# Kernel optimization log

Measured on AMD Instinct MI355X. Metric: run time of the kernel, lower is better.

Reference implementation:

```python
import jax, jax.numpy as jnp
import numpy as np

NUM_HEADS = 16
ROPE_BASE = 10000.0


def _rope_tables(head_dim, seq_len, dtype=jnp.float32):
    # Half-split convention: rotate first half against second half.
    inv_freq = 1.0 / (ROPE_BASE ** (jnp.arange(0, head_dim, 2, dtype=dtype) / head_dim))
    pos = jnp.arange(seq_len, dtype=dtype)
    angles_half = jnp.einsum('s,d->sd', pos, inv_freq)          # (S, D/2)
    angles = jnp.concatenate([angles_half, angles_half], -1)     # (S, D)
    return jnp.cos(angles), jnp.sin(angles)


def _apply_rope(x, cos, sin):
    # x: (H, S, D); cos/sin: (S, D) broadcast over heads
    half = x.shape[-1] // 2
    x1, x2 = x[..., :half], x[..., half:]
    x_rot = jnp.concatenate([-x2, x1], axis=-1)
    return x * cos + x_rot * sin


def setup_inputs() -> dict:
    key = jax.random.key(0)
    S, E = 2048, 2048
    ks = jax.random.split(key, 9)
    sc = 0.02
    return {
        'x': jax.random.normal(ks[0], (S, E), jnp.float32),
        'Wq': jax.random.normal(ks[1], (E, E), jnp.float32) * sc,
        'bq': jax.random.normal(ks[2], (E,), jnp.float32) * sc,
        'Wk': jax.random.normal(ks[3], (E, E), jnp.float32) * sc,
        'bk': jax.random.normal(ks[4], (E,), jnp.float32) * sc,
        'Wv': jax.random.normal(ks[5], (E, E), jnp.float32) * sc,
        'bv': jax.random.normal(ks[6], (E,), jnp.float32) * sc,
        'Wo': jax.random.normal(ks[7], (E, E), jnp.float32) * sc,
        'bo': jax.random.normal(ks[8], (E,), jnp.float32) * sc,
    }


def reference(x, Wq, bq, Wk, bk, Wv, bv, Wo, bo):
    S, E = x.shape
    H = NUM_HEADS
    D = E // H
    scale = D ** 0.5
    cos, sin = _rope_tables(D, S, x.dtype)

    def proj(W, b):
        return (x @ W.T + b).reshape(S, H, D).transpose(1, 0, 2)  # (H, S, D)

    q = _apply_rope(proj(Wq, bq), cos, sin)
    k = _apply_rope(proj(Wk, bk), cos, sin)
    v = proj(Wv, bv)

    scores = jnp.einsum('hsd,htd->hst', q, k) / scale  # (H, S, S)
    attn = jax.nn.softmax(scores, axis=-1)
    out = jnp.einsum('hst,htd->hsd', attn, v)          # (H, S, D)
    # Faithful to the original's transpose(0,1).view(S,E) on a (1,H,S,D)
    # tensor: an in-order (head-major) flatten reinterpreted as (S, E).
    out = out.reshape(S, E)
    return out @ Wo.T + bo
```

## Files before the change

kernel.cpp:

```cpp
#include <hip/hip_runtime.h>

#define SDIM 2048
#define EDIM 2048
#define NHEAD 16
#define DHEAD 128

typedef __attribute__((ext_vector_type(8))) short short8;
typedef __attribute__((ext_vector_type(4))) float floatx4;

__device__ __forceinline__ float bf2f(ushort u) {
    union { uint i; float f; } v; v.i = ((uint)u) << 16; return v.f;
}
__device__ __forceinline__ ushort f2bf(float f) {
    union { float f; uint i; } v; v.f = f;
    uint r = v.i + 0x7fff + ((v.i >> 16) & 1);
    return (ushort)(r >> 16);
}

__device__ __forceinline__ void gload_lds16(const ushort* g, ushort* l) {
    __builtin_amdgcn_global_load_lds(
        (const __attribute__((address_space(1))) void*)g,
        (__attribute__((address_space(3))) void*)l, 16, 0, 0);
}

__global__ void convert5_kernel(
    const float* __restrict__ s0, const float* __restrict__ s1,
    const float* __restrict__ s2, const float* __restrict__ s3,
    const float* __restrict__ s4,
    ushort* __restrict__ d0, ushort* __restrict__ d1,
    ushort* __restrict__ d2, ushort* __restrict__ d3,
    ushort* __restrict__ d4)
{
    const float* src; ushort* dst;
    switch (blockIdx.y) {
        case 0: src = s0; dst = d0; break;
        case 1: src = s1; dst = d1; break;
        case 2: src = s2; dst = d2; break;
        case 3: src = s3; dst = d3; break;
        default: src = s4; dst = d4; break;
    }
    int i = blockIdx.x * blockDim.x + threadIdx.x;
    float4 f = ((const float4*)src)[i];
    ushort4 o;
    o.x = f2bf(f.x); o.y = f2bf(f.y); o.z = f2bf(f.z); o.w = f2bf(f.w);
    ((ushort4*)dst)[i] = o;
}

#define QPRESCALE 0.12754245f

__global__ __launch_bounds__(512, 2) void gemm256_qkv(
    const ushort* __restrict__ A,
    const ushort* __restrict__ B0, const ushort* __restrict__ B1, const ushort* __restrict__ B2,
    const float* __restrict__ s0, const float* __restrict__ s1, const float* __restrict__ s2,
    ushort* __restrict__ C0, ushort* __restrict__ C1, ushort* __restrict__ Vtg)
{
    __shared__ __align__(16) ushort smem[2][2][2][128 * 64];

    const int tid  = threadIdx.x;
    const int lane = tid & 63;
    const int wave = tid >> 6;
    const int l15 = lane & 15, quad = lane >> 4, l7 = lane & 7;
    const int wm = wave & 1, wn = wave >> 1;
    const int bm = blockIdx.x * 256;
    const int which = blockIdx.y >> 3;
    const int n0 = (blockIdx.y & 7) * 256;
    const int NT = EDIM / 64;

    const ushort* Bsel = (which == 0) ? B0 : (which == 1) ? B1 : B2;
    const float*  bia  = (which == 0) ? s0 : (which == 1) ? s1 : s2;

    const int srow = tid >> 3;
    const int sgc  = (((tid & 7) ^ ((tid >> 3) & 7)) << 3);

    floatx4 acc[8][4];
#pragma unroll
    for (int i = 0; i < 8; i++)
#pragma unroll
        for (int j = 0; j < 4; j++) acc[i][j] = (floatx4)0.0f;

    auto stageA = [&](int tile, int h) {
        const ushort* g = A + (size_t)(bm + h * 128 + srow) * EDIM + tile * 64 + sgc;
        ushort* l = &smem[tile & 1][0][h][0] + tid * 8;
        gload_lds16(g, l);
        gload_lds16(g + (size_t)64 * EDIM, l + 4096);
    };
    auto stageB = [&](int tile, int h) {
        const ushort* g = Bsel + (size_t)(n0 + h * 128 + srow) * EDIM + tile * 64 + sgc;
        ushort* l = &smem[tile & 1][1][h][0] + tid * 8;
        gload_lds16(g, l);
        gload_lds16(g + (size_t)64 * EDIM, l + 4096);
    };

    stageA(0, 0); stageA(0, 1); stageB(0, 0); stageB(0, 1);
    stageB(1, 0); stageB(1, 1);
    asm volatile("s_waitcnt vmcnt(4)" ::: "memory");
    __builtin_amdgcn_s_barrier();

    const int c0 = ((quad ^ l7) << 3);
    const int c1 = (((quad + 4) ^ l7) << 3);
    const int brow0 = (wn & 1) * 64;

    short8 af[4], b0[4], b1[4];

#define MFMA16(AOFF, AF, BF) \
    _Pragma("unroll") \
    for (int mf = 0; mf < 4; mf++) \
        _Pragma("unroll") \
        for (int an = 0; an < 4; an++) \
            acc[(AOFF) + mf][an] = __builtin_amdgcn_mfma_f32_16x16x32_bf16( \
                AF[mf], BF[an], acc[(AOFF) + mf][an], 0, 0, 0);

#define PH_PRE() do { \
    asm volatile("" ::: "memory"); \
    __builtin_amdgcn_s_barrier(); \
    asm volatile("s_waitcnt lgkmcnt(0)" ::: "memory"); \
    __builtin_amdgcn_sched_barrier(0); \
    __builtin_amdgcn_s_setprio(1); \
} while (0)
#define PH_POST() do { \
    __builtin_amdgcn_s_setprio(0); \
    asm volatile("" ::: "memory"); \
    __builtin_amdgcn_s_barrier(); \
} while (0)

    for (int t = 0; t < NT; ++t) {
        const ushort* aH = &smem[t & 1][0][wm][0];
        const ushort* bH = &smem[t & 1][1][wn >> 1][0];

#pragma unroll
        for (int mf = 0; mf < 4; mf++)
            af[mf] = *(const short8*)(aH + (mf * 16 + l15) * 64 + c0);
#pragma unroll
        for (int an = 0; an < 4; an++)
            b0[an] = *(const short8*)(bH + (brow0 + an * 16 + l15) * 64 + c0);
        if (t + 1 < NT) stageA(t + 1, 0);
        PH_PRE();
        MFMA16(0, af, b0);
        PH_POST();

        short8 ag[4];
#pragma unroll
        for (int mf = 0; mf < 4; mf++)
            ag[mf] = *(const short8*)(aH + (mf * 16 + l15) * 64 + c1);
#pragma unroll
        for (int an = 0; an < 4; an++)
            b1[an] = *(const short8*)(bH + (brow0 + an * 16 + l15) * 64 + c1);
        if (t + 1 < NT) stageA(t + 1, 1);
        PH_PRE();
        MFMA16(0, ag, b1);
        PH_POST();

#pragma unroll
        for (int mf = 0; mf < 4; mf++)
            af[mf] = *(const short8*)(aH + (64 + mf * 16 + l15) * 64 + c0);
        if (t + 2 < NT) stageB(t + 2, 0);
        PH_PRE();
        MFMA16(4, af, b0);
        PH_POST();

#pragma unroll
        for (int mf = 0; mf < 4; mf++)
            ag[mf] = *(const short8*)(aH + (64 + mf * 16 + l15) * 64 + c1);
        if (t + 2 < NT) stageB(t + 2, 1);
        asm volatile("" ::: "memory");
        __builtin_amdgcn_s_barrier();
        asm volatile("s_waitcnt lgkmcnt(0)" ::: "memory");
        __builtin_amdgcn_sched_barrier(0);
        __builtin_amdgcn_s_setprio(1);
        MFMA16(4, ag, b1);
        __builtin_amdgcn_s_setprio(0);
        if (t < NT - 2) asm volatile("s_waitcnt vmcnt(4)" ::: "memory");
        else            asm volatile("s_waitcnt vmcnt(0)" ::: "memory");
        __builtin_amdgcn_s_barrier();
    }
#undef MFMA16
#undef PH_PRE
#undef PH_POST

    if (which == 2) {
#pragma unroll
        for (int an = 0; an < 4; an++) {
            int col = n0 + wn * 64 + an * 16 + l15;
            int h = col >> 7, d = col & 127;
            float bv = bia[col];
            ushort* cp = Vtg + (size_t)h * SDIM * DHEAD + (size_t)d * SDIM;
#pragma unroll
            for (int am = 0; am < 8; am++) {
                int s = bm + wm * 128 + am * 16 + quad * 4;
                ushort4 pk;
                pk.x = f2bf(acc[am][an][0] + bv);
                pk.y = f2bf(acc[am][an][1] + bv);
                pk.z = f2bf(acc[am][an][2] + bv);
                pk.w = f2bf(acc[am][an][3] + bv);
                *(ushort4*)(cp + s) = pk;
            }
        }
    } else {
        ushort* C = (which == 0) ? C0 : C1;
        const float psc = (which == 0) ? QPRESCALE : 1.0f;
        float* xch = (float*)smem;
        float bv[4], invf[4];
#pragma unroll
        for (int an = 0; an < 4; an++) {
            bv[an]   = bia[n0 + wn * 64 + an * 16 + l15];
            invf[an] = __expf((float)(an * 16 + l15) * -0.14391157f);
        }
        const int mybase = wave * 1024 + quad * 16 + l15;
        const int pbase  = (wave ^ 2) * 1024 + quad * 16 + l15;
        const int rowb = bm + wm * 128 + quad * 4;
#pragma unroll
        for (int am2 = 0; am2 < 4; am2++) {
            __syncthreads();
#pragma unroll
            for (int sl = 0; sl < 2; sl++) {
                int am = am2 * 2 + sl;
#pragma unroll
                for (int an = 0; an < 4; an++)
#pragma unroll
                    for (int r = 0; r < 4; r++)
                        xch[sl * 8192 + mybase + an * 256 + r * 64] = acc[am][an][r] + bv[an];
            }
            __syncthreads();
#pragma unroll
            for (int sl = 0; sl < 2; sl++) {
                int am = am2 * 2 + sl;
#pragma unroll
                for (int an = 0; an < 4; an++) {
                    int col = n0 + wn * 64 + an * 16 + l15;
#pragma unroll
                    for (int r = 0; r < 4; r++) {
                        int row = rowb + am * 16 + r;
                        float v = acc[am][an][r] + bv[an];
                        float w = xch[sl * 8192 + pbase + an * 256 + r * 64];
                        float ang = (float)row * invf[an];
                        float rev = ang * 0.15915494309f;
                        rev -= floorf(rev);
                        float arad = rev * 6.28318530718f;
                        float sn = __sinf(arad), cs = __cosf(arad);
                        float o = ((wn & 1) == 0) ? (v * cs - w * sn) : (v * cs + w * sn);
                        C[(size_t)row * EDIM + col] = f2bf(o * psc);
                    }
                }
            }
        }
    }
}

template <typename OUTT, int KSPLIT>
__global__ __launch_bounds__(256) void gemm_bt(
    const ushort* __restrict__ A,
    const ushort* __restrict__ B0, const ushort* __restrict__ B1, const ushort* __restrict__ B2,
    const float* __restrict__ s0, const float* __restrict__ s1, const float* __restrict__ s2,
    OUTT* __restrict__ C0, OUTT* __restrict__ C1, OUTT* __restrict__ C2,
    int nbpm)
{
    __shared__ __align__(16) ushort smem[2 * 128 * 32];
    ushort* a_s = smem;
    ushort* b_s = smem + 128 * 32;

    const int tid = threadIdx.x;
    const int wave = tid >> 6, lane = tid & 63;
    const int l15 = lane & 15, quad = lane >> 4;
    const int wm = wave & 1, wn = wave >> 1;
    const int bm = blockIdx.x * 128;
    const int which = blockIdx.y / nbpm;
    const int n0 = (blockIdx.y % nbpm) * 128;

    const ushort* B;
    const float*  bia;
    OUTT*         C;
    const ushort* Abase;
    if constexpr (KSPLIT == 2) {
        B = B0; bia = s0; C = C0;
        Abase = A + which * (EDIM / 2);
    } else {
        B   = (which == 0) ? B0 : (which == 1) ? B1 : B2;
        bia = (which == 0) ? s0 : (which == 1) ? s1 : s2;
        C   = (which == 0) ? C0 : (which == 1) ? C1 : C2;
        Abase = A;
    }
    const ushort* Bbase = (KSPLIT == 2) ? B + which * (EDIM / 2) : B;

    floatx4 acc[4][4];
#pragma unroll
    for (int i = 0; i < 4; i++)
#pragma unroll
        for (int j = 0; j < 4; j++) acc[i][j] = (floatx4)0.0f;

    const int t1 = tid + 256;
    const int row0 = tid >> 2, kc0 = (tid & 3) * 8;
    const int row1 = t1 >> 2,  kc1 = (t1 & 3) * 8;

    for (int k0 = 0; k0 < EDIM / KSPLIT; k0 += 32) {
        __syncthreads();
        gload_lds16(Abase + (size_t)(bm + row0) * EDIM + k0 + kc0, a_s + tid * 8);
        gload_lds16(Abase + (size_t)(bm + row1) * EDIM + k0 + kc1, a_s + t1 * 8);
        gload_lds16(Bbase + (size_t)(n0 + row0) * EDIM + k0 + kc0, b_s + tid * 8);
        gload_lds16(Bbase + (size_t)(n0 + row1) * EDIM + k0 + kc1, b_s + t1 * 8);
        __syncthreads();

        short8 af[4], bf[4];
#pragma unroll
        for (int mt = 0; mt < 4; mt++)
            af[mt] = *(const short8*)(a_s + (wm * 64 + mt * 16 + l15) * 32 + quad * 8);
#pragma unroll
        for (int nt = 0; nt < 4; nt++)
            bf[nt] = *(const short8*)(b_s + (wn * 64 + nt * 16 + l15) * 32 + quad * 8);
#pragma unroll
        for (int mt = 0; mt < 4; mt++)
#pragma unroll
            for (int nt = 0; nt < 4; nt++)
                acc[mt][nt] = __builtin_amdgcn_mfma_f32_16x16x32_bf16(af[mt], bf[nt], acc[mt][nt], 0, 0, 0);
    }

    if constexpr (KSPLIT == 2) {
#pragma unroll
        for (int nt = 0; nt < 4; nt++) {
            int col = n0 + wn * 64 + nt * 16 + l15;
            float bv = (which == 0) ? bia[col] : 0.0f;
#pragma unroll
            for (int mt = 0; mt < 4; mt++) {
#pragma unroll
                for (int r = 0; r < 4; r++) {
                    int row = bm + wm * 64 + mt * 16 + quad * 4 + r;
                    atomicAdd(&((float*)C)[(size_t)row * EDIM + col], acc[mt][nt][r] + bv);
                }
            }
        }
    } else {
#pragma unroll
        for (int nt = 0; nt < 4; nt++) {
            int col = n0 + wn * 64 + nt * 16 + l15;
            float bv = bia[col];
#pragma unroll
            for (int mt = 0; mt < 4; mt++) {
#pragma unroll
                for (int r = 0; r < 4; r++) {
                    int row = bm + wm * 64 + mt * 16 + quad * 4 + r;
                    float v = acc[mt][nt][r] + bv;
                    if constexpr (sizeof(OUTT) == 2)
                        ((ushort*)C)[(size_t)row * EDIM + col] = f2bf(v);
                    else
                        ((float*)C)[(size_t)row * EDIM + col] = v;
                }
            }
        }
    }
}

#define MFIX2 17.31234049f
__global__ __launch_bounds__(256, 4) void attn_kernel(
    const ushort* __restrict__ Q, const ushort* __restrict__ K,
    const ushort* __restrict__ Vtg,
    ushort* __restrict__ Opart, float* __restrict__ Lsum,
    ushort* __restrict__ Ab, int nsplit)
{
    __shared__ __align__(16) ushort Ks[64 * 128];
    __shared__ __align__(16) ushort Vt[128 * 64];
    __shared__ __align__(16) ushort Ps[64 * 64];

    const int bid = blockIdx.x;
    const int head = bid & 15, qt = (bid >> 4) & 31, half = bid >> 9;
    const int tid = threadIdx.x, wave = tid >> 6, lane = tid & 63;
    const int l15 = lane & 15, quad = lane >> 4;
    const int l7 = l15 & 7;
    const int kstart = half * (SDIM / nsplit);
    const int ntile = (SDIM / nsplit) / 64;

    short8 qf[4];
    {
        int s = qt * 64 + wave * 16 + l15;
        const ushort* qp = Q + (size_t)s * EDIM + head * DHEAD;
#pragma unroll
        for (int kc = 0; kc < 4; kc++) qf[kc] = *(const short8*)(qp + kc * 32 + quad * 8);
    }

    floatx4 o[8];
#pragma unroll
    for (int i = 0; i < 8; i++) o[i] = (floatx4)0.0f;
    float lsum = 0.0f;

    const int krow = tid >> 4, kc8 = tid & 15;
    const int vd = tid >> 3, vc8 = tid & 7;
    const int prow = wave * 16 + l15;

    for (int kv = 0; kv < ntile; kv++) {
        const int k0 = kstart + kv * 64;
        __syncthreads();
#pragma unroll
        for (int i = 0; i < 4; i++) {
            int row = krow + i * 16;
            uint4 v = *(const uint4*)(K + (size_t)(k0 + row) * EDIM + head * DHEAD + kc8 * 8);
            *(uint4*)(Ks + row * 128 + ((kc8 ^ (row & 7)) << 3)) = v;
        }
#pragma unroll
        for (int i = 0; i < 4; i++) {
            int d = vd + i * 32;
            uint4 v = *(const uint4*)(Vtg + (size_t)head * SDIM * DHEAD + (size_t)d * SDIM + k0 + vc8 * 8);
            *(uint4*)(Vt + d * 64 + ((vc8 ^ (d & 7)) << 3)) = v;
        }
        __syncthreads();

#pragma unroll
        for (int nt = 0; nt < 4; nt++) {
            floatx4 st = (floatx4)0.0f;
            __builtin_amdgcn_s_setprio(1);
#pragma unroll
            for (int kc = 0; kc < 4; kc++) {
                short8 kfr = *(const short8*)(Ks + (nt * 16 + l15) * 128 + (((kc * 4 + quad) ^ l7) << 3));
                st = __builtin_amdgcn_mfma_f32_16x16x32_bf16(kfr, qf[kc], st, 0, 0, 0);
            }
            __builtin_amdgcn_s_setprio(0);
            ushort4 pk;
            float p0 = __builtin_amdgcn_exp2f(st[0] - MFIX2);
            float p1 = __builtin_amdgcn_exp2f(st[1] - MFIX2);
            float p2 = __builtin_amdgcn_exp2f(st[2] - MFIX2);
            float p3 = __builtin_amdgcn_exp2f(st[3] - MFIX2);
            lsum += (p0 + p1) + (p2 + p3);
            pk.x = f2bf(p0); pk.y = f2bf(p1); pk.z = f2bf(p2); pk.w = f2bf(p3);
            int c2 = (nt * 2 + (quad >> 1)) ^ l7;
            *(ushort4*)(Ps + prow * 64 + (c2 << 3) + ((quad & 1) << 2)) = pk;
        }

        __builtin_amdgcn_s_setprio(1);
#pragma unroll
        for (int kc2 = 0; kc2 < 2; kc2++) {
            short8 af = *(const short8*)(Ps + prow * 64 + (((kc2 * 4 + quad) ^ l7) << 3));
#pragma unroll
            for (int nt2 = 0; nt2 < 8; nt2++) {
                short8 bfr = *(const short8*)(Vt + (nt2 * 16 + l15) * 64 + (((kc2 * 4 + quad) ^ l7) << 3));
                o[nt2] = __builtin_amdgcn_mfma_f32_16x16x32_bf16(af, bfr, o[nt2], 0, 0, 0);
            }
        }
        __builtin_amdgcn_s_setprio(0);
    }

    lsum += __shfl_xor(lsum, 16);
    lsum += __shfl_xor(lsum, 32);

    if (nsplit == 1) {
        float invl[4];
#pragma unroll
        for (int r = 0; r < 4; r++) invl[r] = 1.0f / __shfl(lsum, quad * 4 + r, 16);
#pragma unroll
        for (int nt2 = 0; nt2 < 8; nt2++) {
#pragma unroll
            for (int r = 0; r < 4; r++) {
                int s = qt * 64 + wave * 16 + quad * 4 + r;
                int d = nt2 * 16 + l15;
                Ab[(size_t)head * SDIM * DHEAD + (size_t)s * DHEAD + d] = f2bf(o[nt2][r] * invl[r]);
            }
        }
    } else {
        size_t pb = ((size_t)half * NHEAD + head) * SDIM * DHEAD;
#pragma unroll
        for (int nt2 = 0; nt2 < 8; nt2++) {
#pragma unroll
            for (int r = 0; r < 4; r++) {
                int s = qt * 64 + wave * 16 + quad * 4 + r;
                int d = nt2 * 16 + l15;
                Opart[pb + (size_t)s * DHEAD + d] = f2bf(o[nt2][r]);
            }
        }
        if (lane < 16)
            Lsum[((size_t)half * NHEAD + head) * SDIM + qt * 64 + wave * 16 + lane] = lsum;
    }
}

__global__ void merge_kernel(const ushort* __restrict__ Opart,
                             const float* __restrict__ Lsum,
                             ushort* __restrict__ Ab)
{
    const int HS = NHEAD * SDIM;
    int t = blockIdx.x * blockDim.x + threadIdx.x;
    int row = t >> 4, c8 = (t & 15) * 8;
    float inv = 1.0f / (Lsum[row] + Lsum[HS + row] + Lsum[2 * HS + row] + Lsum[3 * HS + row]);
    float acc[8] = {0, 0, 0, 0, 0, 0, 0, 0};
#pragma unroll
    for (int p = 0; p < 4; p++) {
        union { uint4 v; ushort u[8]; } a;
        a.v = *(const uint4*)(Opart + (size_t)p * HS * DHEAD + (size_t)row * DHEAD + c8);
#pragma unroll
        for (int j = 0; j < 8; j++) acc[j] += bf2f(a.u[j]);
    }
    union { uint4 v; ushort u[8]; } ro;
#pragma unroll
    for (int j = 0; j < 8; j++) ro.u[j] = f2bf(acc[j] * inv);
    *(uint4*)(Ab + (size_t)row * DHEAD + c8) = ro.v;
}

extern "C" void kernel_launch(void* const* d_in, const int* in_sizes, int n_in,
                              void* d_out, int out_size, void* d_ws, size_t ws_size,
                              hipStream_t stream) {
    (void)in_sizes; (void)n_in; (void)out_size;
    const float* x  = (const float*)d_in[0];
    const float* Wq = (const float*)d_in[1];
    const float* bq = (const float*)d_in[2];
    const float* Wk = (const float*)d_in[3];
    const float* bk = (const float*)d_in[4];
    const float* Wv = (const float*)d_in[5];
    const float* bv = (const float*)d_in[6];
    const float* Wo = (const float*)d_in[7];
    const float* bo = (const float*)d_in[8];
    float* out = (float*)d_out;

    char* ws = (char*)d_ws;
    const size_t SEG = (size_t)EDIM * EDIM * 2;
    ushort* xb  = (ushort*)(ws + 0 * SEG);
    ushort* Wqb = (ushort*)(ws + 1 * SEG);
    ushort* Wkb = (ushort*)(ws + 2 * SEG);
    ushort* Wvb = (ushort*)(ws + 3 * SEG);
    ushort* Wob = (ushort*)(ws + 4 * SEG);
    ushort* Qb  = (ushort*)(ws + 5 * SEG);
    ushort* Kb  = (ushort*)(ws + 6 * SEG);
    ushort* Vtg = (ushort*)(ws + 7 * SEG);
    ushort* Ab  = (ushort*)(ws + 8 * SEG);
    ushort* Op  = (ushort*)(ws + 0 * SEG);
    float*  Ls  = (float*)(ws + 11 * SEG);

    const int split = (ws_size >= ((size_t)89 << 20)) ? 1 : 0;

    convert5_kernel<<<dim3(4096, 5), 256, 0, stream>>>(
        x, Wq, Wk, Wv, Wo, xb, Wqb, Wkb, Wvb, Wob);

    gemm256_qkv<<<dim3(8, 24), 512, 0, stream>>>(
        xb, Wqb, Wkb, Wvb, bq, bk, bv, Qb, Kb, Vtg);

    if (split) {
        attn_kernel<<<2048, 256, 0, stream>>>(Qb, Kb, Vtg, Op, Ls, Ab, 4);
        merge_kernel<<<2048, 256, 0, stream>>>(Op, Ls, Ab);
        hipMemsetAsync(out, 0, (size_t)EDIM * EDIM * 4, stream);
        gemm_bt<float, 2><<<dim3(16, 32), 256, 0, stream>>>(
            Ab, Wob, Wob, Wob, bo, bo, bo, out, out, out, 16);
    } else {
        attn_kernel<<<512, 256, 0, stream>>>(Qb, Kb, Vtg, Op, Ls, Ab, 1);
        gemm_bt<float, 1><<<dim3(16, 16), 256, 0, stream>>>(
            Ab, Wob, Wob, Wob, bo, bo, bo, out, out, out, 16);
    }
}
```

Before: 298.9 us.

## Fold Wo conversion into QKV GEMM grid and halve attention KV split

Wo's fp32-to-bf16 conversion moves out of the standalone convert kernel and into 64 extra blocks of the QKV GEMM launch, so it can run on CUs left idle by the 192-block GEMM grid. Separately, the attention KV split drops from 4 to 2 partitions, halving the partial outputs and the reads in the merge step while giving the attention launch fewer, longer blocks. The extra GEMM blocks need the same large LDS allocation, and fewer attention blocks may reduce occupancy.

```diff
diff --git a/kernel.cpp b/kernel.cpp
--- a/kernel.cpp
+++ b/kernel.cpp
@@ -23,21 +23,18 @@
         (__attribute__((address_space(3))) void*)l, 16, 0, 0);
 }
 
-__global__ void convert5_kernel(
+__global__ void convert4_kernel(
     const float* __restrict__ s0, const float* __restrict__ s1,
     const float* __restrict__ s2, const float* __restrict__ s3,
-    const float* __restrict__ s4,
     ushort* __restrict__ d0, ushort* __restrict__ d1,
-    ushort* __restrict__ d2, ushort* __restrict__ d3,
-    ushort* __restrict__ d4)
+    ushort* __restrict__ d2, ushort* __restrict__ d3)
 {
     const float* src; ushort* dst;
     switch (blockIdx.y) {
         case 0: src = s0; dst = d0; break;
         case 1: src = s1; dst = d1; break;
         case 2: src = s2; dst = d2; break;
-        case 3: src = s3; dst = d3; break;
-        default: src = s4; dst = d4; break;
+        default: src = s3; dst = d3; break;
     }
     int i = blockIdx.x * blockDim.x + threadIdx.x;
     float4 f = ((const float4*)src)[i];
@@ -52,11 +49,27 @@
     const ushort* __restrict__ A,
     const ushort* __restrict__ B0, const ushort* __restrict__ B1, const ushort* __restrict__ B2,
     const float* __restrict__ s0, const float* __restrict__ s1, const float* __restrict__ s2,
-    ushort* __restrict__ C0, ushort* __restrict__ C1, ushort* __restrict__ Vtg)
+    ushort* __restrict__ C0, ushort* __restrict__ C1, ushort* __restrict__ Vtg,
+    const float* __restrict__ WoF, ushort* __restrict__ WoB)
 {
     __shared__ __align__(16) ushort smem[2][2][2][128 * 64];
 
     const int tid  = threadIdx.x;
+
+    if (blockIdx.y >= 24) {
+        const int idx = (blockIdx.y - 24) * 8 + blockIdx.x;
+        const float4* src = (const float4*)WoF;
+#pragma unroll
+        for (int it = 0; it < 32; ++it) {
+            int i = idx * 16384 + it * 512 + tid;
+            float4 f = src[i];
+            ushort4 o;
+            o.x = f2bf(f.x); o.y = f2bf(f.y); o.z = f2bf(f.z); o.w = f2bf(f.w);
+            ((ushort4*)WoB)[i] = o;
+        }
+        return;
+    }
+
     const int lane = tid & 63;
     const int wave = tid >> 6;
     const int l15 = lane & 15, quad = lane >> 4, l7 = lane & 7;
@@ -474,10 +487,10 @@
     const int HS = NHEAD * SDIM;
     int t = blockIdx.x * blockDim.x + threadIdx.x;
     int row = t >> 4, c8 = (t & 15) * 8;
-    float inv = 1.0f / (Lsum[row] + Lsum[HS + row] + Lsum[2 * HS + row] + Lsum[3 * HS + row]);
+    float inv = 1.0f / (Lsum[row] + Lsum[HS + row]);
     float acc[8] = {0, 0, 0, 0, 0, 0, 0, 0};
 #pragma unroll
-    for (int p = 0; p < 4; p++) {
+    for (int p = 0; p < 2; p++) {
         union { uint4 v; ushort u[8]; } a;
         a.v = *(const uint4*)(Opart + (size_t)p * HS * DHEAD + (size_t)row * DHEAD + c8);
 #pragma unroll
@@ -520,14 +533,14 @@
 
     const int split = (ws_size >= ((size_t)89 << 20)) ? 1 : 0;
 
-    convert5_kernel<<<dim3(4096, 5), 256, 0, stream>>>(
-        x, Wq, Wk, Wv, Wo, xb, Wqb, Wkb, Wvb, Wob);
-
-    gemm256_qkv<<<dim3(8, 24), 512, 0, stream>>>(
-        xb, Wqb, Wkb, Wvb, bq, bk, bv, Qb, Kb, Vtg);
+    convert4_kernel<<<dim3(4096, 4), 256, 0, stream>>>(
+        x, Wq, Wk, Wv, xb, Wqb, Wkb, Wvb);
+
+    gemm256_qkv<<<dim3(8, 32), 512, 0, stream>>>(
+        xb, Wqb, Wkb, Wvb, bq, bk, bv, Qb, Kb, Vtg, Wo, Wob);
 
     if (split) {
-        attn_kernel<<<2048, 256, 0, stream>>>(Qb, Kb, Vtg, Op, Ls, Ab, 4);
+        attn_kernel<<<1024, 256, 0, stream>>>(Qb, Kb, Vtg, Op, Ls, Ab, 2);
         merge_kernel<<<2048, 256, 0, stream>>>(Op, Ls, Ab);
         hipMemsetAsync(out, 0, (size_t)EDIM * EDIM * 4, stream);
         gemm_bt<float, 2><<<dim3(16, 32), 256, 0, stream>>>(
```

Result: no change. 293.7 us, median of 2 (-1.7%).
